# Optimization experiments

Measured on AMD Instinct MI355X. Metric: run time of the kernel, lower is better.

Reference implementation:

```python
import jax, jax.numpy as jnp
import numpy as np

NPOINT, NSAMPLE, RADIUS = 1024, 32, 0.2
EPS = 1e-5


def fps(xyz, npoint):
    # furthest point sampling: sequential over npoint steps (inherent recurrence)
    B, N, _ = xyz.shape

    def step(carry, _):
        dists, cur = carry
        last = jnp.take_along_axis(xyz, cur[:, None, None], axis=1)[:, 0]  # (B,3)
        d = jnp.sum((xyz - last[:, None, :]) ** 2, axis=-1)  # (B,N)
        dists = jnp.minimum(dists, d)
        nxt = jnp.argmax(dists, axis=-1).astype(jnp.int32)
        return (dists, nxt), cur

    init = (jnp.full((B, N), 1e10, xyz.dtype), jnp.zeros((B,), jnp.int32))
    _, idx = jax.lax.scan(step, init, None, length=npoint)
    return idx.T  # (B, npoint)


def ball_query(xyz, new_xyz, radius, nsample):
    # first `nsample` points (in index order) within radius of each query
    B, N, _ = xyz.shape
    d2 = jnp.sum((new_xyz[:, :, None, :] - xyz[:, None, :, :]) ** 2, -1)  # (B,P,N)
    mask = d2 < radius * radius
    key = jnp.where(mask, jnp.arange(N, dtype=jnp.int32), jnp.int32(N))
    negv, ord_ = jax.lax.top_k(-key, nsample)  # smallest keys = earliest valid idx
    valid = (-negv) < N
    first = ord_[..., :1]  # query point itself is always in-radius
    return jnp.where(valid, ord_, first)  # (B, P, nsample) int32


def bn_relu(x, g, b):
    # BatchNorm2d training-mode stats over (B, P, S) per channel, then ReLU
    m = jnp.mean(x, axis=(0, 1, 2))
    v = jnp.var(x, axis=(0, 1, 2))
    return jax.nn.relu((x - m) * jax.lax.rsqrt(v + EPS) * g + b)


def sa_forward(xyz, features, W1, g1, b1, W2, g2, b2, W3, g3, b3):
    B, N, _ = xyz.shape
    fps_idx = fps(xyz, NPOINT)  # (B,P)
    new_xyz = jnp.take_along_axis(xyz, fps_idx[:, :, None], axis=1)  # (B,P,3)
    idx = ball_query(xyz, new_xyz, RADIUS, NSAMPLE)  # (B,P,S)

    gather = jax.vmap(lambda pts, i: pts[i])  # per-batch irregular gather
    grouped_xyz = gather(xyz, idx) - new_xyz[:, :, None, :]  # (B,P,S,3)
    grouped_feat = gather(jnp.swapaxes(features, 1, 2), idx)  # (B,P,S,C)
    h = jnp.concatenate([grouped_xyz, grouped_feat], axis=-1)  # (B,P,S,3+C)

    # shared MLP = 1x1 Conv2d (no bias) + BN + ReLU, three layers
    h = bn_relu(jnp.einsum('bpsc,oc->bpso', h, W1), g1, b1)
    h = bn_relu(jnp.einsum('bpsc,oc->bpso', h, W2), g2, b2)
    h = bn_relu(jnp.einsum('bpsc,oc->bpso', h, W3), g3, b3)

    new_features = jnp.max(h, axis=2)  # max-pool over nsample -> (B,P,Cout)
    return new_xyz, jnp.swapaxes(new_features, 1, 2)  # (B,P,3), (B,Cout,P)


def setup_inputs() -> dict:
    key = jax.random.key(0)
    ks = jax.random.split(key, 6)
    B, N, C = 16, 4096, 64
    return {
        'xyz': jax.random.uniform(ks[0], (B, N, 3), jnp.float32),
        'features': jax.random.normal(ks[1], (B, C, N), jnp.float32),
        'W1': jax.random.normal(ks[2], (64, 67), jnp.float32) * 0.1,
        'g1': jnp.ones((64,), jnp.float32), 'b1': jnp.zeros((64,), jnp.float32),
        'W2': jax.random.normal(ks[3], (64, 64), jnp.float32) * 0.1,
        'g2': jnp.ones((64,), jnp.float32), 'b2': jnp.zeros((64,), jnp.float32),
        'W3': jax.random.normal(ks[4], (128, 64), jnp.float32) * 0.1,
        'g3': jnp.ones((128,), jnp.float32), 'b3': jnp.zeros((128,), jnp.float32),
    }


def reference(xyz, features, W1, g1, b1, W2, g2, b2, W3, g3, b3):
    return sa_forward(xyz, features, W1, g1, b1, W2, g2, b2, W3, g3, b3)
```

## Files before the change

kernel.cpp:

```cpp
#include <hip/hip_runtime.h>

#define NN 4096
#define NPOINTS 1024
#define NSAMP 32
#define MROWS (16*NPOINTS*NSAMP)
#define NPAIRS (MROWS/32)
#define OUT2_OFF (16*NPOINTS*3)
#define EPSF 1e-5f
#define RPB 128
#define NBLK 4096

typedef unsigned long long ull;
using f32x4  = __attribute__((ext_vector_type(4))) float;
using bf16x8 = __attribute__((ext_vector_type(8))) short;

__device__ __forceinline__ float bflo(unsigned int u){ union{unsigned int i; float f;} v; v.i = u << 16; return v.f; }
__device__ __forceinline__ float bfhi(unsigned int u){ union{unsigned int i; float f;} v; v.i = u & 0xffff0000u; return v.f; }
__device__ __forceinline__ unsigned short f2bf(float f){
  union{float f; unsigned int i;} v; v.f = f;
  unsigned int r = v.i + 0x7fffu + ((v.i >> 16) & 1u);
  return (unsigned short)(r >> 16);
}

__global__ __launch_bounds__(512) void k_fps(const float* __restrict__ xyz,
    float* __restrict__ nxyz, float* __restrict__ out){
  __shared__ float xs[NN], ys[NN], zs[NN];
  __shared__ ull wbest[2][8];
  const int b = blockIdx.x, t = threadIdx.x;
  const float* xb = xyz + (size_t)b*NN*3;
  for (int j = t; j < NN; j += 512){
    xs[j] = xb[j*3+0]; ys[j] = xb[j*3+1]; zs[j] = xb[j*3+2];
  }
  __syncthreads();
  float px[8], py[8], pz[8], pd[8];
  #pragma unroll
  for (int j=0;j<8;j++){ int i=j*512+t; px[j]=xs[i]; py[j]=ys[i]; pz[j]=zs[i]; pd[j]=1e10f; }
  int cur = 0;
  const int lane = t & 63, wv = t >> 6;
  for (int it=0; it<NPOINTS; ++it){
    float lx = xs[cur], ly = ys[cur], lz = zs[cur];
    if (t == 0){
      int o = (b*NPOINTS + it)*3;
      nxyz[o]=lx; nxyz[o+1]=ly; nxyz[o+2]=lz;
      out[o]=lx;  out[o+1]=ly;  out[o+2]=lz;
    }
    float bv = -1.0f; int bi = 0;
    #pragma unroll
    for (int j=0;j<8;j++){
      float dx = __fsub_rn(px[j], lx);
      float dy = __fsub_rn(py[j], ly);
      float dz = __fsub_rn(pz[j], lz);
      float d  = __fadd_rn(__fadd_rn(__fmul_rn(dx,dx), __fmul_rn(dy,dy)), __fmul_rn(dz,dz));
      float nd = fminf(pd[j], d);
      pd[j] = nd;
      if (nd > bv){ bv = nd; bi = j*512 + t; }
    }
    ull key = ((ull)__float_as_uint(bv) << 32) | (ull)(0xFFFFFFFFu - (unsigned)bi);
    #define DPPSTEP(ctrl, rmask) { \
      unsigned int tlo = __builtin_amdgcn_update_dpp(0, (int)(unsigned int)(key & 0xFFFFFFFFull), ctrl, rmask, 0xf, false); \
      unsigned int thi = __builtin_amdgcn_update_dpp(0, (int)(unsigned int)(key >> 32), ctrl, rmask, 0xf, false); \
      ull tk = ((ull)thi << 32) | (ull)tlo; \
      if (tk > key) key = tk; }
    DPPSTEP(0x111, 0xf)
    DPPSTEP(0x112, 0xf)
    DPPSTEP(0x114, 0xf)
    DPPSTEP(0x118, 0xf)
    DPPSTEP(0x142, 0xa)
    DPPSTEP(0x143, 0xc)
    #undef DPPSTEP
    if (lane == 63) wbest[it & 1][wv] = key;
    __syncthreads();
    ull best = wbest[it & 1][0];
    #pragma unroll
    for (int w=1; w<8; w++){
      ull ok = wbest[it & 1][w];
      if (ok > best) best = ok;
    }
    cur = (int)(0xFFFFFFFFu - (unsigned)(best & 0xFFFFFFFFull));
  }
}

__global__ __launch_bounds__(256) void k_ball(const float* __restrict__ xyz,
    const float* __restrict__ nxyz, int* __restrict__ ball_idx){
  const int lane = threadIdx.x & 63;
  const int q = blockIdx.x*4 + (threadIdx.x >> 6);
  const int b = q >> 10;
  const float* xb = xyz + (size_t)b*NN*3;
  const int co = q*3;
  const float cx = nxyz[co], cy = nxyz[co+1], cz = nxyz[co+2];
  const int base = q*NSAMP;
  const float R2 = 0.04f;
  int cnt = 0, first = 0;
  for (int i0 = 0; i0 < NN; i0 += 64){
    const int i = i0 + lane;
    float lx = xb[i*3+0], ly = xb[i*3+1], lz = xb[i*3+2];
    float dx = __fsub_rn(cx, lx);
    float dy = __fsub_rn(cy, ly);
    float dz = __fsub_rn(cz, lz);
    float d2 = __fadd_rn(__fadd_rn(__fmul_rn(dx,dx), __fmul_rn(dy,dy)), __fmul_rn(dz,dz));
    const bool in = (d2 < R2);
    ull mask = __ballot(in);
    if (mask){
      if (cnt == 0) first = i0 + (int)__ffsll((long long)mask) - 1;
      int slot = cnt + (int)__popcll(mask & ((1ull << lane) - 1ull));
      if (in && slot < NSAMP) ball_idx[base + slot] = i;
      cnt += (int)__popcll(mask);
      if (cnt >= NSAMP) break;
    }
  }
  if (lane >= cnt && lane < NSAMP) ball_idx[base + lane] = first;
}

__device__ __forceinline__ unsigned short packhl(float v, int isLo){
  unsigned short h = f2bf(v);
  if (isLo){ float r = __fsub_rn(v, bflo((unsigned)h)); h = f2bf(r); }
  return h;
}

__global__ __launch_bounds__(256) void k_wt(const float* __restrict__ W1, const float* __restrict__ W2,
    const float* __restrict__ W3, float* __restrict__ W1T, float* __restrict__ W2T, float* __restrict__ W3T,
    unsigned short* __restrict__ w1p, unsigned short* __restrict__ w2p, unsigned short* __restrict__ w3p){
  int t = blockIdx.x*256 + threadIdx.x;
  if (t < 67*64){ int c = t >> 6, o = t & 63;  W1T[t] = W1[o*67 + c]; }
  if (t < 64*64){ int c = t >> 6, o = t & 63;  W2T[t] = W2[o*64 + c]; }
  if (t < 64*128){ int c = t >> 7, o = t & 127; W3T[t] = W3[o*64 + c]; }
  if (t < 1024){
    int f=t>>6, l=t&63, isLo=f>>3, f0=f&7, kf=f0>>2, ntg=f0&3;
    const float* src = W1 + (ntg*16+(l&15))*67 + 3 + kf*32 + ((l>>4)*8);
    unsigned short* dst = w1p + ((size_t)f*64 + l)*8;
    #pragma unroll
    for (int j=0;j<8;j++) dst[j] = packhl(src[j], isLo);
  }
  if (t < 1024){
    int f=t>>6, l=t&63, isLo=f>>3, f0=f&7, kf=f0>>2, ntg=f0&3;
    const float* src = W2 + (ntg*16+(l&15))*64 + kf*32 + ((l>>4)*8);
    unsigned short* dst = w2p + ((size_t)f*64 + l)*8;
    #pragma unroll
    for (int j=0;j<8;j++) dst[j] = packhl(src[j], isLo);
  }
  if (t < 2048){
    int f=t>>6, l=t&63, isLo=f>>4, f0=f&15, kf=f0>>3, ntg=f0&7;
    const float* src = W3 + (ntg*16+(l&15))*64 + kf*32 + ((l>>4)*8);
    unsigned short* dst = w3p + ((size_t)f*64 + l)*8;
    #pragma unroll
    for (int j=0;j<8;j++) dst[j] = packhl(src[j], isLo);
  }
}

__global__ __launch_bounds__(256) void k_ft(const float* __restrict__ feat, unsigned short* __restrict__ featT){
  __shared__ float tile[64][65];
  const int b = blockIdx.x >> 6, n0 = (blockIdx.x & 63) << 6;
  const int t = threadIdx.x;
  const int nl = t & 63, cb = t >> 6;
  #pragma unroll
  for (int k=0;k<16;k++){
    int c = cb + (k<<2);
    tile[c][nl] = feat[((size_t)(b*64 + c))*NN + n0 + nl];
  }
  __syncthreads();
  #pragma unroll
  for (int k=0;k<16;k++){
    int nl2 = cb + (k<<2);
    featT[((size_t)(b*NN) + n0 + nl2)*64 + nl] = f2bf(tile[nl][nl2]);
  }
}

__device__ __forceinline__ void gather_y1(int r,
    const float* __restrict__ xyz, const unsigned short* __restrict__ featT,
    const float* __restrict__ nxyz, const int* __restrict__ ball_idx,
    const float* __restrict__ W1T, float* __restrict__ y)
{
  const int b = r >> 15;
  const int p = (r >> 5) & (NPOINTS-1);
  const int i = ball_idx[r];
  const int co = (b*NPOINTS + p)*3;
  const float* xp = xyz + ((size_t)(b*NN + i))*3;
  const float h0 = __fsub_rn(xp[0], nxyz[co]);
  const float h1 = __fsub_rn(xp[1], nxyz[co+1]);
  const float h2 = __fsub_rn(xp[2], nxyz[co+2]);
  #pragma unroll
  for (int o=0;o<64;o++) y[o] = h0 * W1T[o];
  #pragma unroll
  for (int o=0;o<64;o++) y[o] = fmaf(h1, W1T[64+o], y[o]);
  #pragma unroll
  for (int o=0;o<64;o++) y[o] = fmaf(h2, W1T[128+o], y[o]);
  const uint4* fp = (const uint4*)(featT + ((size_t)(b*NN + i))*64);
  #pragma unroll
  for (int c8=0;c8<8;c8++){
    const uint4 u = fp[c8];
    float fv[8];
    fv[0]=bflo(u.x); fv[1]=bfhi(u.x); fv[2]=bflo(u.y); fv[3]=bfhi(u.y);
    fv[4]=bflo(u.z); fv[5]=bfhi(u.z); fv[6]=bflo(u.w); fv[7]=bfhi(u.w);
    const float* wb = W1T + (3 + c8*8)*64;
    #pragma unroll
    for (int k=0;k<8;k++){
      #pragma unroll
      for (int o=0;o<64;o++) y[o] = fmaf(fv[k], wb[k*64+o], y[o]);
    }
  }
}

__device__ __forceinline__ void load_act(const unsigned short* __restrict__ act, int r, float* __restrict__ y){
  const uint4* p = (const uint4*)(act + (size_t)r*64);
  #pragma unroll
  for (int j=0;j<8;j++){
    uint4 u = p[j];
    y[j*8+0]=bflo(u.x); y[j*8+1]=bfhi(u.x); y[j*8+2]=bflo(u.y); y[j*8+3]=bfhi(u.y);
    y[j*8+4]=bflo(u.z); y[j*8+5]=bfhi(u.z); y[j*8+6]=bflo(u.w); y[j*8+7]=bfhi(u.w);
  }
}

__device__ __forceinline__ void store_bf16x64(unsigned short* __restrict__ dst, const float* __restrict__ y){
  uint4* row = (uint4*)dst;
  #pragma unroll
  for (int j=0;j<8;j++){
    union { uint4 u; unsigned short h[8]; } pk;
    #pragma unroll
    for (int k=0;k<8;k++) pk.h[k] = f2bf(y[j*8+k]);
    row[j] = pk.u;
  }
}

__device__ __forceinline__ void bnrelu64(float* __restrict__ y,
    const float* __restrict__ sc, const float* __restrict__ sh){
  #pragma unroll
  for (int o=0;o<64;o++) y[o] = fmaxf(0.f, fmaf(y[o], sc[o], sh[o]));
}

template<int LDW>
__device__ __forceinline__ void gemm64(const float* __restrict__ a, const float* __restrict__ WT,
                                       float* __restrict__ out){
  #pragma unroll
  for (int o=0;o<64;o++) out[o] = 0.f;
  #pragma unroll 4
  for (int c=0;c<64;c++){
    const float av = a[c];
    const float* wb = WT + c*LDW;
    #pragma unroll
    for (int o=0;o<64;o++) out[o] = fmaf(av, wb[o], out[o]);
  }
}

__device__ __forceinline__ void stats_tile(float* tile, int t, const float* __restrict__ y,
                                           float& s, float& q){
  #pragma unroll
  for (int j=0;j<64;j++) tile[t*65 + j] = y[j];
  __syncthreads();
  #pragma unroll 8
  for (int r=0;r<64;r++){
    float v = tile[r*65 + t];
    s += v; q = fmaf(v, v, q);
  }
  __syncthreads();
}

template<int STAGE, int SRC, bool STORE>
__global__ __launch_bounds__(64) void k_stage(
    const float* __restrict__ xyz, const unsigned short* __restrict__ featT,
    const float* __restrict__ nxyz, const int* __restrict__ ball_idx,
    const unsigned short* __restrict__ actin, unsigned short* __restrict__ actout,
    const float* __restrict__ W1T, const float* __restrict__ W2T, const float* __restrict__ W3T,
    const float* __restrict__ sc1, const float* __restrict__ sh1,
    const float* __restrict__ sc2, const float* __restrict__ sh2,
    float* __restrict__ sums)
{
  __shared__ float tile[64*65];
  const int t = threadIdx.x;
  float s0=0.f, q0=0.f, s1=0.f, q1=0.f;
  for (int it=0; it<RPB/64; ++it){
    const int r = blockIdx.x*RPB + it*64 + t;
    float y[64];
    if constexpr (SRC == 0) gather_y1(r, xyz, featT, nxyz, ball_idx, W1T, y);
    else                    load_act(actin, r, y);
    if constexpr (STAGE == 1){
      if constexpr (STORE) store_bf16x64(actout + (size_t)r*64, y);
      stats_tile(tile, t, y, s0, q0);
    } else if constexpr (STAGE == 2){
      bnrelu64(y, sc1, sh1);
      float y2[64];
      gemm64<64>(y, W2T, y2);
      if constexpr (STORE) store_bf16x64(actout + (size_t)r*64, y2);
      stats_tile(tile, t, y2, s0, q0);
    } else {
      float a2[64];
      if constexpr (SRC != 2){
        bnrelu64(y, sc1, sh1);
        gemm64<64>(y, W2T, a2);
      } else {
        #pragma unroll
        for (int o=0;o<64;o++) a2[o] = y[o];
      }
      bnrelu64(a2, sc2, sh2);
      float y3[64];
      gemm64<128>(a2, W3T, y3);
      if constexpr (STORE) store_bf16x64(actout + (size_t)r*128, y3);
      stats_tile(tile, t, y3, s0, q0);
      gemm64<128>(a2, W3T + 64, y3);
      if constexpr (STORE) store_bf16x64(actout + (size_t)r*128 + 64, y3);
      stats_tile(tile, t, y3, s1, q1);
    }
  }
  if constexpr (STAGE < 3){
    atomicAdd(&sums[t], s0);
    atomicAdd(&sums[64 + t], q0);
  } else {
    atomicAdd(&sums[t], s0);
    atomicAdd(&sums[64 + t], s1);
    atomicAdd(&sums[128 + t], q0);
    atomicAdd(&sums[192 + t], q1);
  }
}

template<int C>
__global__ void k_fin(const float* __restrict__ sums,
    const float* __restrict__ g, const float* __restrict__ bv,
    float* __restrict__ scale, float* __restrict__ shift)
{
  const int c = threadIdx.x;
  float m  = sums[c]   * (1.f/(float)MROWS);
  float vv = sums[C+c] * (1.f/(float)MROWS) - m*m;
  float sc = g[c] / sqrtf(vv + EPSF);
  scale[c] = sc;
  shift[c] = bv[c] - m*sc;
}

__global__ __launch_bounds__(256) void k_mg1(
    const float* __restrict__ xyz, const unsigned short* __restrict__ featT,
    const float* __restrict__ nxyz, const int* __restrict__ ball_idx,
    const unsigned short* __restrict__ w1p, const float* __restrict__ W1T,
    unsigned short* __restrict__ act1, float* __restrict__ sums)
{
  __shared__ float hxs[256], hys[256], hzs[256];
  __shared__ float w1s[192];
  __shared__ float lsum[128];
  const int t = threadIdx.x, lane = t & 63, wv = t >> 6;
  const int blkrow = blockIdx.x*256;
  {
    int r = blkrow + t;
    int b = r >> 15, p = (r >> 5) & (NPOINTS-1), i = ball_idx[r];
    const float* xp = xyz + ((size_t)(b*NN + i))*3;
    int co = (b*NPOINTS + p)*3;
    hxs[t] = __fsub_rn(xp[0], nxyz[co]);
    hys[t] = __fsub_rn(xp[1], nxyz[co+1]);
    hzs[t] = __fsub_rn(xp[2], nxyz[co+2]);
  }
  if (t < 192) w1s[t] = W1T[t];
  if (t < 128) lsum[t] = 0.f;
  __syncthreads();
  const int rowbase = blkrow + wv*64;
  const int kc0 = (lane>>4)*8;
  bf16x8 A[4][2];
  #pragma unroll
  for (int mt=0;mt<4;mt++){
    int r = rowbase + mt*16 + (lane&15);
    int b = r >> 15, i = ball_idx[r];
    const unsigned short* fp = featT + ((size_t)(b*NN + i))*64 + kc0;
    A[mt][0] = *(const bf16x8*)(fp);
    A[mt][1] = *(const bf16x8*)(fp + 32);
  }
  bf16x8 Bh[2][4], Bl[2][4];
  #pragma unroll
  for (int kf=0;kf<2;kf++)
    #pragma unroll
    for (int nt=0;nt<4;nt++){
      Bh[kf][nt] = *(const bf16x8*)(w1p + ((size_t)(kf*4+nt)*64 + lane)*8);
      Bl[kf][nt] = *(const bf16x8*)(w1p + ((size_t)(8 + kf*4+nt)*64 + lane)*8);
    }
  f32x4 c[4][4];
  const int lr0 = wv*64 + (lane>>4)*4;
  #pragma unroll
  for (int nt=0;nt<4;nt++){
    int col = nt*16 + (lane&15);
    float w0 = w1s[col], w1 = w1s[64+col], w2 = w1s[128+col];
    #pragma unroll
    for (int mt=0;mt<4;mt++)
      #pragma unroll
      for (int rr=0;rr<4;rr++){
        int lr = lr0 + mt*16 + rr;
        c[mt][nt][rr] = fmaf(hzs[lr], w2, fmaf(hys[lr], w1, hxs[lr]*w0));
      }
  }
  #pragma unroll
  for (int mt=0;mt<4;mt++)
    #pragma unroll
    for (int nt=0;nt<4;nt++){
      f32x4 acc = c[mt][nt];
      acc = __builtin_amdgcn_mfma_f32_16x16x32_bf16(A[mt][0], Bh[0][nt], acc, 0,0,0);
      acc = __builtin_amdgcn_mfma_f32_16x16x32_bf16(A[mt][1], Bh[1][nt], acc, 0,0,0);
      acc = __builtin_amdgcn_mfma_f32_16x16x32_bf16(A[mt][0], Bl[0][nt], acc, 0,0,0);
      acc = __builtin_amdgcn_mfma_f32_16x16x32_bf16(A[mt][1], Bl[1][nt], acc, 0,0,0);
      c[mt][nt] = acc;
    }
  #pragma unroll
  for (int nt=0;nt<4;nt++){
    float s=0.f, q=0.f;
    #pragma unroll
    for (int mt=0;mt<4;mt++)
      #pragma unroll
      for (int rr=0;rr<4;rr++){ float v=c[mt][nt][rr]; s+=v; q=fmaf(v,v,q); }
    s += __shfl_xor(s,16,64); s += __shfl_xor(s,32,64);
    q += __shfl_xor(q,16,64); q += __shfl_xor(q,32,64);
    if (lane<16){
      atomicAdd(&lsum[nt*16+lane], s);
      atomicAdd(&lsum[64 + nt*16+lane], q);
    }
  }
  #pragma unroll
  for (int nt=0;nt<4;nt++)
    #pragma unroll
    for (int mt=0;mt<4;mt++)
      #pragma unroll
      for (int rr=0;rr<4;rr++){
        int row = rowbase + mt*16 + (lane>>4)*4 + rr;
        act1[(size_t)row*64 + nt*16 + (lane&15)] = f2bf(c[mt][nt][rr]);
      }
  __syncthreads();
  if (t < 128) atomicAdd(&sums[t], lsum[t]);
}

__device__ __forceinline__ bf16x8 ldA_bn(const unsigned short* __restrict__ p,
    const float* __restrict__ sc, const float* __restrict__ sh){
  uint4 u = *(const uint4*)p;
  unsigned w[4] = {u.x, u.y, u.z, u.w};
  union { bf16x8 v; unsigned short h[8]; } o;
  #pragma unroll
  for (int q=0;q<4;q++){
    float lo = fmaxf(0.f, fmaf(bflo(w[q]), sc[2*q],   sh[2*q]));
    float hi = fmaxf(0.f, fmaf(bfhi(w[q]), sc[2*q+1], sh[2*q+1]));
    o.h[2*q]   = f2bf(lo);
    o.h[2*q+1] = f2bf(hi);
  }
  return o.v;
}

template<int NOUT, bool MINMAX>
__global__ __launch_bounds__(256) void k_mgemm(
    const unsigned short* __restrict__ actin,
    unsigned short* __restrict__ actout,
    const unsigned short* __restrict__ wp,
    const float* __restrict__ scp, const float* __restrict__ shp,
    float* __restrict__ sums,
    float* __restrict__ ymax, float* __restrict__ ymin)
{
  constexpr int NTG = NOUT/16;
  __shared__ float lsum[2*NOUT];
  const int t = threadIdx.x, lane = t & 63, wv = t >> 6;
  for (int i=t;i<2*NOUT;i+=256) lsum[i]=0.f;
  __syncthreads();
  const int rowbase = blockIdx.x*256 + wv*64;
  const int kc0 = (lane>>4)*8;
  float scl[16], shl[16];
  #pragma unroll
  for (int kf=0;kf<2;kf++)
    #pragma unroll
    for (int j=0;j<8;j++){
      scl[kf*8+j] = scp[kf*32+kc0+j];
      shl[kf*8+j] = shp[kf*32+kc0+j];
    }
  bf16x8 A[4][2];
  #pragma unroll
  for (int mt=0;mt<4;mt++)
    #pragma unroll
    for (int kf=0;kf<2;kf++)
      A[mt][kf] = ldA_bn(actin + ((size_t)(rowbase + mt*16 + (lane&15)))*64 + kf*32 + kc0,
                         &scl[kf*8], &shl[kf*8]);
  #pragma unroll
  for (int h=0; h<NOUT/64; h++){
    bf16x8 Bh[2][4], Bl[2][4];
    #pragma unroll
    for (int kf=0;kf<2;kf++)
      #pragma unroll
      for (int nt=0;nt<4;nt++){
        int ntg = h*4+nt;
        Bh[kf][nt] = *(const bf16x8*)(wp + ((size_t)(kf*NTG+ntg)*64 + lane)*8);
        Bl[kf][nt] = *(const bf16x8*)(wp + ((size_t)(2*NTG + kf*NTG+ntg)*64 + lane)*8);
      }
    f32x4 c[4][4];
    #pragma unroll
    for (int mt=0;mt<4;mt++)
      #pragma unroll
      for (int nt=0;nt<4;nt++){
        f32x4 acc = {0.f,0.f,0.f,0.f};
        acc = __builtin_amdgcn_mfma_f32_16x16x32_bf16(A[mt][0], Bh[0][nt], acc, 0,0,0);
        acc = __builtin_amdgcn_mfma_f32_16x16x32_bf16(A[mt][1], Bh[1][nt], acc, 0,0,0);
        acc = __builtin_amdgcn_mfma_f32_16x16x32_bf16(A[mt][0], Bl[0][nt], acc, 0,0,0);
        acc = __builtin_amdgcn_mfma_f32_16x16x32_bf16(A[mt][1], Bl[1][nt], acc, 0,0,0);
        c[mt][nt] = acc;
      }
    #pragma unroll
    for (int nt=0;nt<4;nt++){
      float s=0.f, q=0.f;
      #pragma unroll
      for (int mt=0;mt<4;mt++)
        #pragma unroll
        for (int r=0;r<4;r++){ float v=c[mt][nt][r]; s+=v; q=fmaf(v,v,q); }
      s += __shfl_xor(s,16,64); s += __shfl_xor(s,32,64);
      q += __shfl_xor(q,16,64); q += __shfl_xor(q,32,64);
      if (lane<16){
        atomicAdd(&lsum[h*64+nt*16+lane], s);
        atomicAdd(&lsum[NOUT + h*64+nt*16+lane], q);
      }
    }
    if constexpr (!MINMAX){
      #pragma unroll
      for (int nt=0;nt<4;nt++)
        #pragma unroll
        for (int mt=0;mt<4;mt++)
          #pragma unroll
          for (int r=0;r<4;r++){
            int row = rowbase + mt*16 + (lane>>4)*4 + r;
            actout[(size_t)row*NOUT + h*64 + nt*16 + (lane&15)] = f2bf(c[mt][nt][r]);
          }
    } else {
      #pragma unroll
      for (int nt=0;nt<4;nt++){
        float mx0=-1e30f, mn0=1e30f, mx1=-1e30f, mn1=1e30f;
        #pragma unroll
        for (int mt=0;mt<2;mt++)
          #pragma unroll
          for (int r=0;r<4;r++){ float v=c[mt][nt][r]; mx0=fmaxf(mx0,v); mn0=fminf(mn0,v); }
        #pragma unroll
        for (int mt=2;mt<4;mt++)
          #pragma unroll
          for (int r=0;r<4;r++){ float v=c[mt][nt][r]; mx1=fmaxf(mx1,v); mn1=fminf(mn1,v); }
        mx0=fmaxf(mx0,__shfl_xor(mx0,16,64)); mx0=fmaxf(mx0,__shfl_xor(mx0,32,64));
        mn0=fminf(mn0,__shfl_xor(mn0,16,64)); mn0=fminf(mn0,__shfl_xor(mn0,32,64));
        mx1=fmaxf(mx1,__shfl_xor(mx1,16,64)); mx1=fmaxf(mx1,__shfl_xor(mx1,32,64));
        mn1=fminf(mn1,__shfl_xor(mn1,16,64)); mn1=fminf(mn1,__shfl_xor(mn1,32,64));
        if (lane<16){
          int ch = h*64+nt*16+lane;
          int pair0 = rowbase>>5;
          float2 vx = {mx0, mx1}, vn = {mn0, mn1};
          *(float2*)(ymax + (size_t)ch*NPAIRS + pair0) = vx;
          *(float2*)(ymin + (size_t)ch*NPAIRS + pair0) = vn;
        }
      }
    }
  }
  __syncthreads();
  for (int i=t;i<2*NOUT;i+=256) atomicAdd(&sums[i], lsum[i]);
}

__global__ __launch_bounds__(256) void k_mx(const float* __restrict__ ymax,
    const float* __restrict__ ymin, const float* __restrict__ sc3,
    const float* __restrict__ sh3, float* __restrict__ out){
  int idx = blockIdx.x*256 + threadIdx.x;
  int p = idx & 1023;
  int o = (idx>>10) & 127;
  int b = idx>>17;
  float sc = sc3[o], sh = sh3[o];
  size_t src = (size_t)o*NPAIRS + b*1024 + p;
  float v = (sc >= 0.f) ? ymax[src] : ymin[src];
  out[OUT2_OFF + ((size_t)(b*128+o))*1024 + p] = fmaxf(0.f, fmaf(v, sc, sh));
}

template<bool FROMACT>
__global__ __launch_bounds__(64) void k_pass2(
    const float* __restrict__ xyz, const unsigned short* __restrict__ featT,
    const float* __restrict__ nxyz, const int* __restrict__ ball_idx,
    const unsigned short* __restrict__ act1,
    const float* __restrict__ W1T, const float* __restrict__ W2T,
    const float* __restrict__ W3,
    const float* __restrict__ sc1, const float* __restrict__ sh1,
    const float* __restrict__ sc2, const float* __restrict__ sh2,
    const float* __restrict__ sc3, const float* __restrict__ sh3,
    float* __restrict__ out)
{
  const int t = threadIdx.x;
  const int s = t & 31;
  const int pair = blockIdx.x*2 + (t >> 5);
  const int r = pair*32 + s;
  float y[64];
  if (FROMACT) load_act(act1, r, y);
  else         gather_y1(r, xyz, featT, nxyz, ball_idx, W1T, y);
  bnrelu64(y, sc1, sh1);
  float a2[64];
  gemm64<64>(y, W2T, a2);
  bnrelu64(a2, sc2, sh2);
  const int b = pair >> 10, p = pair & (NPOINTS-1);
  float* ob = out + OUT2_OFF + ((size_t)b*128)*1024 + p;
  for (int o=0;o<128;o++){
    const float* wr = W3 + o*64;
    float v = 0.f;
    #pragma unroll
    for (int c=0;c<64;c++) v = fmaf(a2[c], wr[c], v);
    v = fmaxf(0.f, fmaf(v, sc3[o], sh3[o]));
    #pragma unroll
    for (int off=16; off>=1; off>>=1) v = fmaxf(v, __shfl_xor(v, off, 64));
    if (s == 0) ob[(size_t)o*1024] = v;
  }
}

extern "C" void kernel_launch(void* const* d_in, const int* in_sizes, int n_in,
                              void* d_out, int out_size, void* d_ws, size_t ws_size,
                              hipStream_t stream) {
  const float* xyz  = (const float*)d_in[0];
  const float* feat = (const float*)d_in[1];
  const float* W1   = (const float*)d_in[2];
  const float* g1   = (const float*)d_in[3];
  const float* b1   = (const float*)d_in[4];
  const float* W2   = (const float*)d_in[5];
  const float* g2   = (const float*)d_in[6];
  const float* b2   = (const float*)d_in[7];
  const float* W3   = (const float*)d_in[8];
  const float* g3   = (const float*)d_in[9];
  const float* b3   = (const float*)d_in[10];
  float* out = (float*)d_out;
  char* ws = (char*)d_ws;

  const size_t o_nxyz = 0;
  const size_t o_ball = o_nxyz + 196608;
  const size_t o_w1t  = o_ball + 2097152;
  const size_t o_w2t  = o_w1t  + 17408;
  const size_t o_w3t  = o_w2t  + 16384;
  const size_t o_w1p  = o_w3t  + 32768;
  const size_t o_w2p  = o_w1p  + 16384;
  const size_t o_w3p  = o_w2p  + 16384;
  const size_t o_bn   = o_w3p  + 32768;
  const size_t o_sum  = o_bn   + 3072;
  const size_t o_ft   = o_sum  + 2048;
  const size_t o_mm   = o_ft   + (size_t)16*NN*64*2;
  const size_t o_act1 = o_mm   + (size_t)2*128*NPAIRS*4;
  const size_t SZ_A64 = (size_t)MROWS*64*2;
  const size_t NEED1  = o_act1 + SZ_A64;
  const size_t o_act2 = o_act1 + SZ_A64;
  const size_t NEED2  = o_act2 + SZ_A64;

  float* nxyz   = (float*)(ws + o_nxyz);
  int*   ball   = (int*)  (ws + o_ball);
  float* W1T    = (float*)(ws + o_w1t);
  float* W2T    = (float*)(ws + o_w2t);
  float* W3T    = (float*)(ws + o_w3t);
  unsigned short* w1p = (unsigned short*)(ws + o_w1p);
  unsigned short* w2p = (unsigned short*)(ws + o_w2p);
  unsigned short* w3p = (unsigned short*)(ws + o_w3p);
  float* sc1    = (float*)(ws + o_bn);
  float* sh1    = (float*)(ws + o_bn + 512);
  float* sc2    = (float*)(ws + o_bn + 1024);
  float* sh2    = (float*)(ws + o_bn + 1536);
  float* sc3    = (float*)(ws + o_bn + 2048);
  float* sh3    = (float*)(ws + o_bn + 2560);
  float* sums1  = (float*)(ws + o_sum);
  float* sums2  = (float*)(ws + o_sum + 512);
  float* sums3  = (float*)(ws + o_sum + 1024);
  unsigned short* featT = (unsigned short*)(ws + o_ft);
  float* ymax   = (float*)(ws + o_mm);
  float* ymin   = (float*)(ws + o_mm + (size_t)128*NPAIRS*4);
  unsigned short* act1  = (unsigned short*)(ws + o_act1);
  unsigned short* act2  = (unsigned short*)(ws + o_act2);

  const int tier = (ws_size >= NEED2) ? 2 : (ws_size >= NEED1) ? 1 : 0;

  hipMemsetAsync(ws + o_sum, 0, 2048, stream);

  k_wt  <<<32,   256, 0, stream>>>(W1, W2, W3, W1T, W2T, W3T, w1p, w2p, w3p);
  k_ft  <<<1024, 256, 0, stream>>>(feat, featT);
  k_fps <<<16,   512, 0, stream>>>(xyz, nxyz, out);
  k_ball<<<4096, 256, 0, stream>>>(xyz, nxyz, ball);

  if (tier == 2){
    k_mg1<<<MROWS/256, 256, 0, stream>>>(xyz, featT, nxyz, ball, w1p, W1T, act1, sums1);
    k_fin<64><<<1, 64, 0, stream>>>(sums1, g1, b1, sc1, sh1);
    k_mgemm<64,false><<<MROWS/256, 256, 0, stream>>>(act1, act2, w2p, sc1, sh1, sums2,
                                                     nullptr, nullptr);
    k_fin<64><<<1, 64, 0, stream>>>(sums2, g2, b2, sc2, sh2);
    k_mgemm<128,true><<<MROWS/256, 256, 0, stream>>>(act2, nullptr, w3p, sc2, sh2, sums3,
                                                     ymax, ymin);
    k_fin<128><<<1, 128, 0, stream>>>(sums3, g3, b3, sc3, sh3);
    k_mx<<<(16*128*1024)/256, 256, 0, stream>>>(ymax, ymin, sc3, sh3, out);
  } else if (tier == 1){
    k_stage<1,0,true><<<NBLK, 64, 0, stream>>>(xyz, featT, nxyz, ball, nullptr, act1,
                                               W1T, W2T, W3T, sc1, sh1, sc2, sh2, sums1);
    k_fin<64><<<1, 64, 0, stream>>>(sums1, g1, b1, sc1, sh1);
    k_stage<2,1,false><<<NBLK, 64, 0, stream>>>(xyz, featT, nxyz, ball, act1, nullptr,
                                                W1T, W2T, W3T, sc1, sh1, sc2, sh2, sums2);
    k_fin<64><<<1, 64, 0, stream>>>(sums2, g2, b2, sc2, sh2);
    k_stage<3,1,false><<<NBLK, 64, 0, stream>>>(xyz, featT, nxyz, ball, act1, nullptr,
                                                W1T, W2T, W3T, sc1, sh1, sc2, sh2, sums3);
    k_fin<128><<<1, 128, 0, stream>>>(sums3, g3, b3, sc3, sh3);
    k_pass2<true><<<8192, 64, 0, stream>>>(xyz, featT, nxyz, ball, act1, W1T, W2T, W3,
                                           sc1, sh1, sc2, sh2, sc3, sh3, out);
  } else {
    k_stage<1,0,false><<<NBLK, 64, 0, stream>>>(xyz, featT, nxyz, ball, nullptr, nullptr,
                                                W1T, W2T, W3T, sc1, sh1, sc2, sh2, sums1);
    k_fin<64><<<1, 64, 0, stream>>>(sums1, g1, b1, sc1, sh1);
    k_stage<2,0,false><<<NBLK, 64, 0, stream>>>(xyz, featT, nxyz, ball, nullptr, nullptr,
                                                W1T, W2T, W3T, sc1, sh1, sc2, sh2, sums2);
    k_fin<64><<<1, 64, 0, stream>>>(sums2, g2, b2, sc2, sh2);
    k_stage<3,0,false><<<NBLK, 64, 0, stream>>>(xyz, featT, nxyz, ball, nullptr, nullptr,
                                                W1T, W2T, W3T, sc1, sh1, sc2, sh2, sums3);
    k_fin<128><<<1, 128, 0, stream>>>(sums3, g3, b3, sc3, sh3);
    k_pass2<false><<<8192, 64, 0, stream>>>(xyz, featT, nxyz, ball, nullptr, W1T, W2T, W3,
                                            sc1, sh1, sc2, sh2, sc3, sh3, out);
  }
}
```

Baseline: 991.3 us.

## Merge FPS, feature transpose and weight packing into one launch

Combines the furthest-point-sampling, feature-transpose and weight-packing kernels into a single launch that dispatches on block index. The other blocks can then run alongside the 16 serial FPS blocks, removing two launches and the serialisation between them. The FPS inner loop is also reworked: it computes the per-thread max with fmaxf over paired points, then recovers the lowest matching index with equality tests, and it skips the reduction on the final iteration. The cost is a larger shared-memory footprint and 512-thread blocks for the transpose and packing work.

```diff
diff --git a/kernel.cpp b/kernel.cpp
--- a/kernel.cpp
+++ b/kernel.cpp
@@ -22,61 +22,136 @@
   return (unsigned short)(r >> 16);
 }
 
-__global__ __launch_bounds__(512) void k_fps(const float* __restrict__ xyz,
-    float* __restrict__ nxyz, float* __restrict__ out){
-  __shared__ float xs[NN], ys[NN], zs[NN];
-  __shared__ ull wbest[2][8];
-  const int b = blockIdx.x, t = threadIdx.x;
-  const float* xb = xyz + (size_t)b*NN*3;
-  for (int j = t; j < NN; j += 512){
-    xs[j] = xb[j*3+0]; ys[j] = xb[j*3+1]; zs[j] = xb[j*3+2];
-  }
-  __syncthreads();
-  float px[8], py[8], pz[8], pd[8];
-  #pragma unroll
-  for (int j=0;j<8;j++){ int i=j*512+t; px[j]=xs[i]; py[j]=ys[i]; pz[j]=zs[i]; pd[j]=1e10f; }
-  int cur = 0;
-  const int lane = t & 63, wv = t >> 6;
-  for (int it=0; it<NPOINTS; ++it){
-    float lx = xs[cur], ly = ys[cur], lz = zs[cur];
-    if (t == 0){
-      int o = (b*NPOINTS + it)*3;
-      nxyz[o]=lx; nxyz[o+1]=ly; nxyz[o+2]=lz;
-      out[o]=lx;  out[o+1]=ly;  out[o+2]=lz;
-    }
-    float bv = -1.0f; int bi = 0;
-    #pragma unroll
-    for (int j=0;j<8;j++){
-      float dx = __fsub_rn(px[j], lx);
-      float dy = __fsub_rn(py[j], ly);
-      float dz = __fsub_rn(pz[j], lz);
-      float d  = __fadd_rn(__fadd_rn(__fmul_rn(dx,dx), __fmul_rn(dy,dy)), __fmul_rn(dz,dz));
-      float nd = fminf(pd[j], d);
-      pd[j] = nd;
-      if (nd > bv){ bv = nd; bi = j*512 + t; }
-    }
-    ull key = ((ull)__float_as_uint(bv) << 32) | (ull)(0xFFFFFFFFu - (unsigned)bi);
-    #define DPPSTEP(ctrl, rmask) { \
-      unsigned int tlo = __builtin_amdgcn_update_dpp(0, (int)(unsigned int)(key & 0xFFFFFFFFull), ctrl, rmask, 0xf, false); \
-      unsigned int thi = __builtin_amdgcn_update_dpp(0, (int)(unsigned int)(key >> 32), ctrl, rmask, 0xf, false); \
-      ull tk = ((ull)thi << 32) | (ull)tlo; \
-      if (tk > key) key = tk; }
-    DPPSTEP(0x111, 0xf)
-    DPPSTEP(0x112, 0xf)
-    DPPSTEP(0x114, 0xf)
-    DPPSTEP(0x118, 0xf)
-    DPPSTEP(0x142, 0xa)
-    DPPSTEP(0x143, 0xc)
-    #undef DPPSTEP
-    if (lane == 63) wbest[it & 1][wv] = key;
+__device__ __forceinline__ unsigned short packhl(float v, int isLo){
+  unsigned short h = f2bf(v);
+  if (isLo){ float r = __fsub_rn(v, bflo((unsigned)h)); h = f2bf(r); }
+  return h;
+}
+
+__global__ __launch_bounds__(512) void k_pre(
+    const float* __restrict__ xyz, const float* __restrict__ feat,
+    const float* __restrict__ W1, const float* __restrict__ W2, const float* __restrict__ W3,
+    float* __restrict__ nxyz, float* __restrict__ out, unsigned short* __restrict__ featT,
+    float* __restrict__ W1T, float* __restrict__ W2T, float* __restrict__ W3T,
+    unsigned short* __restrict__ w1p, unsigned short* __restrict__ w2p, unsigned short* __restrict__ w3p)
+{
+  __shared__ float smem[3*NN + 64];
+  const int bid = blockIdx.x;
+  const int t = threadIdx.x;
+
+  if (bid < 16){
+    float* xs = smem; float* ys = smem + NN; float* zs = smem + 2*NN;
+    ull* wbest = (ull*)(smem + 3*NN);
+    const int b = bid;
+    const float* xb = xyz + (size_t)b*NN*3;
+    for (int j = t; j < NN; j += 512){
+      xs[j] = xb[j*3+0]; ys[j] = xb[j*3+1]; zs[j] = xb[j*3+2];
+    }
     __syncthreads();
-    ull best = wbest[it & 1][0];
-    #pragma unroll
-    for (int w=1; w<8; w++){
-      ull ok = wbest[it & 1][w];
-      if (ok > best) best = ok;
-    }
-    cur = (int)(0xFFFFFFFFu - (unsigned)(best & 0xFFFFFFFFull));
+    float2 px[4], py[4], pz[4], pd[4];
+    #pragma unroll
+    for (int j=0;j<4;j++){
+      int i0 = (2*j)*512 + t, i1 = (2*j+1)*512 + t;
+      px[j] = make_float2(xs[i0], xs[i1]);
+      py[j] = make_float2(ys[i0], ys[i1]);
+      pz[j] = make_float2(zs[i0], zs[i1]);
+      pd[j] = make_float2(1e10f, 1e10f);
+    }
+    int cur = 0;
+    const int lane = t & 63, wv = t >> 6;
+    for (int it=0; it<NPOINTS; ++it){
+      float lx = xs[cur], ly = ys[cur], lz = zs[cur];
+      if (t == 0){
+        int o = (b*NPOINTS + it)*3;
+        nxyz[o]=lx; nxyz[o+1]=ly; nxyz[o+2]=lz;
+        out[o]=lx;  out[o+1]=ly;  out[o+2]=lz;
+      }
+      if (it == NPOINTS-1) break;
+      float2 bv2 = make_float2(-1.0f, -1.0f);
+      #pragma unroll
+      for (int j=0;j<4;j++){
+        float dxx = __fsub_rn(px[j].x, lx), dxy = __fsub_rn(px[j].y, lx);
+        float dyx = __fsub_rn(py[j].x, ly), dyy = __fsub_rn(py[j].y, ly);
+        float dzx = __fsub_rn(pz[j].x, lz), dzy = __fsub_rn(pz[j].y, lz);
+        float dX = __fadd_rn(__fadd_rn(__fmul_rn(dxx,dxx), __fmul_rn(dyx,dyx)), __fmul_rn(dzx,dzx));
+        float dY = __fadd_rn(__fadd_rn(__fmul_rn(dxy,dxy), __fmul_rn(dyy,dyy)), __fmul_rn(dzy,dzy));
+        float ndX = fminf(pd[j].x, dX), ndY = fminf(pd[j].y, dY);
+        pd[j].x = ndX; pd[j].y = ndY;
+        bv2.x = fmaxf(bv2.x, ndX);
+        bv2.y = fmaxf(bv2.y, ndY);
+      }
+      float bv = fmaxf(bv2.x, bv2.y);
+      int bi = 0;
+      #pragma unroll
+      for (int j=3;j>=0;j--){
+        if (pd[j].y == bv) bi = (2*j+1)*512 + t;
+        if (pd[j].x == bv) bi = (2*j)*512 + t;
+      }
+      ull key = ((ull)__float_as_uint(bv) << 32) | (ull)(0xFFFFFFFFu - (unsigned)bi);
+      #define DPPSTEP(ctrl, rmask) { \
+        unsigned int tlo = __builtin_amdgcn_update_dpp(0, (int)(unsigned int)(key & 0xFFFFFFFFull), ctrl, rmask, 0xf, false); \
+        unsigned int thi = __builtin_amdgcn_update_dpp(0, (int)(unsigned int)(key >> 32), ctrl, rmask, 0xf, false); \
+        ull tk = ((ull)thi << 32) | (ull)tlo; \
+        if (tk > key) key = tk; }
+      DPPSTEP(0x111, 0xf)
+      DPPSTEP(0x112, 0xf)
+      DPPSTEP(0x114, 0xf)
+      DPPSTEP(0x118, 0xf)
+      DPPSTEP(0x142, 0xa)
+      DPPSTEP(0x143, 0xc)
+      #undef DPPSTEP
+      if (lane == 63) wbest[(it & 1)*8 + wv] = key;
+      __syncthreads();
+      ull best = wbest[(it & 1)*8];
+      #pragma unroll
+      for (int w=1; w<8; w++){
+        ull ok = wbest[(it & 1)*8 + w];
+        if (ok > best) best = ok;
+      }
+      cur = (int)(0xFFFFFFFFu - (unsigned)(best & 0xFFFFFFFFull));
+    }
+  } else if (bid < 16 + 1024){
+    float* tile = smem;
+    const int fb = bid - 16;
+    const int b = fb >> 6, n0 = (fb & 63) << 6;
+    const int nl = t & 63, cb = t >> 6;
+    #pragma unroll
+    for (int k=0;k<8;k++){
+      int c = cb + (k<<3);
+      tile[c*65 + nl] = feat[((size_t)(b*64 + c))*NN + n0 + nl];
+    }
+    __syncthreads();
+    #pragma unroll
+    for (int k=0;k<8;k++){
+      int nl2 = cb + (k<<3);
+      featT[((size_t)(b*NN) + n0 + nl2)*64 + nl] = f2bf(tile[nl*65 + nl2]);
+    }
+  } else {
+    int g = (bid - 1040)*512 + t;
+    if (g < 67*64){ int c = g >> 6, o = g & 63;  W1T[g] = W1[o*67 + c]; }
+    if (g < 64*64){ int c = g >> 6, o = g & 63;  W2T[g] = W2[o*64 + c]; }
+    if (g < 64*128){ int c = g >> 7, o = g & 127; W3T[g] = W3[o*64 + c]; }
+    if (g < 1024){
+      int f=g>>6, l=g&63, isLo=f>>3, f0=f&7, kf=f0>>2, ntg=f0&3;
+      const float* src = W1 + (ntg*16+(l&15))*67 + 3 + kf*32 + ((l>>4)*8);
+      unsigned short* dst = w1p + ((size_t)f*64 + l)*8;
+      #pragma unroll
+      for (int j=0;j<8;j++) dst[j] = packhl(src[j], isLo);
+    }
+    if (g < 1024){
+      int f=g>>6, l=g&63, isLo=f>>3, f0=f&7, kf=f0>>2, ntg=f0&3;
+      const float* src = W2 + (ntg*16+(l&15))*64 + kf*32 + ((l>>4)*8);
+      unsigned short* dst = w2p + ((size_t)f*64 + l)*8;
+      #pragma unroll
+      for (int j=0;j<8;j++) dst[j] = packhl(src[j], isLo);
+    }
+    if (g < 2048){
+      int f=g>>6, l=g&63, isLo=f>>4, f0=f&15, kf=f0>>3, ntg=f0&7;
+      const float* src = W3 + (ntg*16+(l&15))*64 + kf*32 + ((l>>4)*8);
+      unsigned short* dst = w3p + ((size_t)f*64 + l)*8;
+      #pragma unroll
+      for (int j=0;j<8;j++) dst[j] = packhl(src[j], isLo);
+    }
   }
 }
 
@@ -109,60 +184,6 @@
     }
   }
   if (lane >= cnt && lane < NSAMP) ball_idx[base + lane] = first;
-}
-
-__device__ __forceinline__ unsigned short packhl(float v, int isLo){
-  unsigned short h = f2bf(v);
-  if (isLo){ float r = __fsub_rn(v, bflo((unsigned)h)); h = f2bf(r); }
-  return h;
-}
-
-__global__ __launch_bounds__(256) void k_wt(const float* __restrict__ W1, const float* __restrict__ W2,
-    const float* __restrict__ W3, float* __restrict__ W1T, float* __restrict__ W2T, float* __restrict__ W3T,
-    unsigned short* __restrict__ w1p, unsigned short* __restrict__ w2p, unsigned short* __restrict__ w3p){
-  int t = blockIdx.x*256 + threadIdx.x;
-  if (t < 67*64){ int c = t >> 6, o = t & 63;  W1T[t] = W1[o*67 + c]; }
-  if (t < 64*64){ int c = t >> 6, o = t & 63;  W2T[t] = W2[o*64 + c]; }
-  if (t < 64*128){ int c = t >> 7, o = t & 127; W3T[t] = W3[o*64 + c]; }
-  if (t < 1024){
-    int f=t>>6, l=t&63, isLo=f>>3, f0=f&7, kf=f0>>2, ntg=f0&3;
-    const float* src = W1 + (ntg*16+(l&15))*67 + 3 + kf*32 + ((l>>4)*8);
-    unsigned short* dst = w1p + ((size_t)f*64 + l)*8;
-    #pragma unroll
-    for (int j=0;j<8;j++) dst[j] = packhl(src[j], isLo);
-  }
-  if (t < 1024){
-    int f=t>>6, l=t&63, isLo=f>>3, f0=f&7, kf=f0>>2, ntg=f0&3;
-    const float* src = W2 + (ntg*16+(l&15))*64 + kf*32 + ((l>>4)*8);
-    unsigned short* dst = w2p + ((size_t)f*64 + l)*8;
-    #pragma unroll
-    for (int j=0;j<8;j++) dst[j] = packhl(src[j], isLo);
-  }
-  if (t < 2048){
-    int f=t>>6, l=t&63, isLo=f>>4, f0=f&15, kf=f0>>3, ntg=f0&7;
-    const float* src = W3 + (ntg*16+(l&15))*64 + kf*32 + ((l>>4)*8);
-    unsigned short* dst = w3p + ((size_t)f*64 + l)*8;
-    #pragma unroll
-    for (int j=0;j<8;j++) dst[j] = packhl(src[j], isLo);
-  }
-}
-
-__global__ __launch_bounds__(256) void k_ft(const float* __restrict__ feat, unsigned short* __restrict__ featT){
-  __shared__ float tile[64][65];
-  const int b = blockIdx.x >> 6, n0 = (blockIdx.x & 63) << 6;
-  const int t = threadIdx.x;
-  const int nl = t & 63, cb = t >> 6;
-  #pragma unroll
-  for (int k=0;k<16;k++){
-    int c = cb + (k<<2);
-    tile[c][nl] = feat[((size_t)(b*64 + c))*NN + n0 + nl];
-  }
-  __syncthreads();
-  #pragma unroll
-  for (int k=0;k<16;k++){
-    int nl2 = cb + (k<<2);
-    featT[((size_t)(b*NN) + n0 + nl2)*64 + nl] = f2bf(tile[nl][nl2]);
-  }
 }
 
 __device__ __forceinline__ void gather_y1(int r,
@@ -653,9 +674,9 @@
 
   hipMemsetAsync(ws + o_sum, 0, 2048, stream);
 
-  k_wt  <<<32,   256, 0, stream>>>(W1, W2, W3, W1T, W2T, W3T, w1p, w2p, w3p);
-  k_ft  <<<1024, 256, 0, stream>>>(feat, featT);
-  k_fps <<<16,   512, 0, stream>>>(xyz, nxyz, out);
+  k_pre <<<16 + 1024 + 32, 512, 0, stream>>>(xyz, feat, W1, W2, W3,
+                                             nxyz, out, featT, W1T, W2T, W3T,
+                                             w1p, w2p, w3p);
   k_ball<<<4096, 256, 0, stream>>>(xyz, nxyz, ball);
 
   if (tier == 2){
```

New measurement: 1.112 ms. +12.2%, slower.

## Merge prep kernels into one launch and fold BN finalize into GEMM tails

Applied to the files above, without the earlier changes.

The weight-pack, feature-transpose and ball-query kernels become one block-indexed kernel launched after FPS. The three separate BN finalize launches are replaced by a last-block-done pattern using atomic counters inside the MLP kernels. The goal is fewer kernel launches and less launch gap on the stream. In exchange, the feature transpose now waits for FPS to finish instead of running before it, and every MLP block pays an extra threadfence and atomic.

```diff
diff --git a/kernel.cpp b/kernel.cpp
--- a/kernel.cpp
+++ b/kernel.cpp
@@ -20,6 +20,12 @@
   union{float f; unsigned int i;} v; v.f = f;
   unsigned int r = v.i + 0x7fffu + ((v.i >> 16) & 1u);
   return (unsigned short)(r >> 16);
+}
+
+__device__ __forceinline__ unsigned short packhl(float v, int isLo){
+  unsigned short h = f2bf(v);
+  if (isLo){ float r = __fsub_rn(v, bflo((unsigned)h)); h = f2bf(r); }
+  return h;
 }
 
 __global__ __launch_bounds__(512) void k_fps(const float* __restrict__ xyz,
@@ -80,88 +86,106 @@
   }
 }
 
-__global__ __launch_bounds__(256) void k_ball(const float* __restrict__ xyz,
-    const float* __restrict__ nxyz, int* __restrict__ ball_idx){
-  const int lane = threadIdx.x & 63;
-  const int q = blockIdx.x*4 + (threadIdx.x >> 6);
-  const int b = q >> 10;
-  const float* xb = xyz + (size_t)b*NN*3;
-  const int co = q*3;
-  const float cx = nxyz[co], cy = nxyz[co+1], cz = nxyz[co+2];
-  const int base = q*NSAMP;
-  const float R2 = 0.04f;
-  int cnt = 0, first = 0;
-  for (int i0 = 0; i0 < NN; i0 += 64){
-    const int i = i0 + lane;
-    float lx = xb[i*3+0], ly = xb[i*3+1], lz = xb[i*3+2];
-    float dx = __fsub_rn(cx, lx);
-    float dy = __fsub_rn(cy, ly);
-    float dz = __fsub_rn(cz, lz);
-    float d2 = __fadd_rn(__fadd_rn(__fmul_rn(dx,dx), __fmul_rn(dy,dy)), __fmul_rn(dz,dz));
-    const bool in = (d2 < R2);
-    ull mask = __ballot(in);
-    if (mask){
-      if (cnt == 0) first = i0 + (int)__ffsll((long long)mask) - 1;
-      int slot = cnt + (int)__popcll(mask & ((1ull << lane) - 1ull));
-      if (in && slot < NSAMP) ball_idx[base + slot] = i;
-      cnt += (int)__popcll(mask);
-      if (cnt >= NSAMP) break;
-    }
-  }
-  if (lane >= cnt && lane < NSAMP) ball_idx[base + lane] = first;
-}
-
-__device__ __forceinline__ unsigned short packhl(float v, int isLo){
-  unsigned short h = f2bf(v);
-  if (isLo){ float r = __fsub_rn(v, bflo((unsigned)h)); h = f2bf(r); }
-  return h;
-}
-
-__global__ __launch_bounds__(256) void k_wt(const float* __restrict__ W1, const float* __restrict__ W2,
-    const float* __restrict__ W3, float* __restrict__ W1T, float* __restrict__ W2T, float* __restrict__ W3T,
-    unsigned short* __restrict__ w1p, unsigned short* __restrict__ w2p, unsigned short* __restrict__ w3p){
-  int t = blockIdx.x*256 + threadIdx.x;
-  if (t < 67*64){ int c = t >> 6, o = t & 63;  W1T[t] = W1[o*67 + c]; }
-  if (t < 64*64){ int c = t >> 6, o = t & 63;  W2T[t] = W2[o*64 + c]; }
-  if (t < 64*128){ int c = t >> 7, o = t & 127; W3T[t] = W3[o*64 + c]; }
-  if (t < 1024){
-    int f=t>>6, l=t&63, isLo=f>>3, f0=f&7, kf=f0>>2, ntg=f0&3;
-    const float* src = W1 + (ntg*16+(l&15))*67 + 3 + kf*32 + ((l>>4)*8);
-    unsigned short* dst = w1p + ((size_t)f*64 + l)*8;
-    #pragma unroll
-    for (int j=0;j<8;j++) dst[j] = packhl(src[j], isLo);
-  }
-  if (t < 1024){
-    int f=t>>6, l=t&63, isLo=f>>3, f0=f&7, kf=f0>>2, ntg=f0&3;
-    const float* src = W2 + (ntg*16+(l&15))*64 + kf*32 + ((l>>4)*8);
-    unsigned short* dst = w2p + ((size_t)f*64 + l)*8;
-    #pragma unroll
-    for (int j=0;j<8;j++) dst[j] = packhl(src[j], isLo);
-  }
-  if (t < 2048){
-    int f=t>>6, l=t&63, isLo=f>>4, f0=f&15, kf=f0>>3, ntg=f0&7;
-    const float* src = W3 + (ntg*16+(l&15))*64 + kf*32 + ((l>>4)*8);
-    unsigned short* dst = w3p + ((size_t)f*64 + l)*8;
-    #pragma unroll
-    for (int j=0;j<8;j++) dst[j] = packhl(src[j], isLo);
-  }
-}
-
-__global__ __launch_bounds__(256) void k_ft(const float* __restrict__ feat, unsigned short* __restrict__ featT){
-  __shared__ float tile[64][65];
-  const int b = blockIdx.x >> 6, n0 = (blockIdx.x & 63) << 6;
+__global__ __launch_bounds__(256) void k_pb(
+    const float* __restrict__ xyz, const float* __restrict__ nxyz, int* __restrict__ ball_idx,
+    const float* __restrict__ feat, unsigned short* __restrict__ featT,
+    const float* __restrict__ W1, const float* __restrict__ W2, const float* __restrict__ W3,
+    float* __restrict__ W1T, float* __restrict__ W2T, float* __restrict__ W3T,
+    unsigned short* __restrict__ w1p, unsigned short* __restrict__ w2p, unsigned short* __restrict__ w3p)
+{
+  __shared__ float tile[64*65];
+  const int bid = blockIdx.x;
   const int t = threadIdx.x;
-  const int nl = t & 63, cb = t >> 6;
-  #pragma unroll
-  for (int k=0;k<16;k++){
-    int c = cb + (k<<2);
-    tile[c][nl] = feat[((size_t)(b*64 + c))*NN + n0 + nl];
-  }
-  __syncthreads();
-  #pragma unroll
-  for (int k=0;k<16;k++){
-    int nl2 = cb + (k<<2);
-    featT[((size_t)(b*NN) + n0 + nl2)*64 + nl] = f2bf(tile[nl][nl2]);
+  if (bid < 1024){
+    const int b = bid >> 6, n0 = (bid & 63) << 6;
+    const int nl = t & 63, cb = t >> 6;
+    #pragma unroll
+    for (int k=0;k<16;k++){
+      int c = cb + (k<<2);
+      tile[c*65 + nl] = feat[((size_t)(b*64 + c))*NN + n0 + nl];
+    }
+    __syncthreads();
+    #pragma unroll
+    for (int k=0;k<16;k++){
+      int nl2 = cb + (k<<2);
+      featT[((size_t)(b*NN) + n0 + nl2)*64 + nl] = f2bf(tile[nl*65 + nl2]);
+    }
+  } else if (bid < 1056){
+    int g = (bid - 1024)*256 + t;
+    if (g < 67*64){ int c = g >> 6, o = g & 63;  W1T[g] = W1[o*67 + c]; }
+    if (g < 64*64){ int c = g >> 6, o = g & 63;  W2T[g] = W2[o*64 + c]; }
+    if (g < 64*128){ int c = g >> 7, o = g & 127; W3T[g] = W3[o*64 + c]; }
+    if (g < 1024){
+      int f=g>>6, l=g&63, isLo=f>>3, f0=f&7, kf=f0>>2, ntg=f0&3;
+      const float* src = W1 + (ntg*16+(l&15))*67 + 3 + kf*32 + ((l>>4)*8);
+      unsigned short* dst = w1p + ((size_t)f*64 + l)*8;
+      #pragma unroll
+      for (int j=0;j<8;j++) dst[j] = packhl(src[j], isLo);
+    }
+    if (g < 1024){
+      int f=g>>6, l=g&63, isLo=f>>3, f0=f&7, kf=f0>>2, ntg=f0&3;
+      const float* src = W2 + (ntg*16+(l&15))*64 + kf*32 + ((l>>4)*8);
+      unsigned short* dst = w2p + ((size_t)f*64 + l)*8;
+      #pragma unroll
+      for (int j=0;j<8;j++) dst[j] = packhl(src[j], isLo);
+    }
+    if (g < 2048){
+      int f=g>>6, l=g&63, isLo=f>>4, f0=f&15, kf=f0>>3, ntg=f0&7;
+      const float* src = W3 + (ntg*16+(l&15))*64 + kf*32 + ((l>>4)*8);
+      unsigned short* dst = w3p + ((size_t)f*64 + l)*8;
+      #pragma unroll
+      for (int j=0;j<8;j++) dst[j] = packhl(src[j], isLo);
+    }
+  } else {
+    const int lane = t & 63;
+    const int q = (bid - 1056)*4 + (t >> 6);
+    const int b = q >> 10;
+    const float* xb = xyz + (size_t)b*NN*3;
+    const int co = q*3;
+    const float cx = nxyz[co], cy = nxyz[co+1], cz = nxyz[co+2];
+    const int base = q*NSAMP;
+    const float R2 = 0.04f;
+    int cnt = 0, first = 0;
+    for (int i0 = 0; i0 < NN; i0 += 64){
+      const int i = i0 + lane;
+      float lx = xb[i*3+0], ly = xb[i*3+1], lz = xb[i*3+2];
+      float dx = __fsub_rn(cx, lx);
+      float dy = __fsub_rn(cy, ly);
+      float dz = __fsub_rn(cz, lz);
+      float d2 = __fadd_rn(__fadd_rn(__fmul_rn(dx,dx), __fmul_rn(dy,dy)), __fmul_rn(dz,dz));
+      const bool in = (d2 < R2);
+      ull mask = __ballot(in);
+      if (mask){
+        if (cnt == 0) first = i0 + (int)__ffsll((long long)mask) - 1;
+        int slot = cnt + (int)__popcll(mask & ((1ull << lane) - 1ull));
+        if (in && slot < NSAMP) ball_idx[base + slot] = i;
+        cnt += (int)__popcll(mask);
+        if (cnt >= NSAMP) break;
+      }
+    }
+    if (lane >= cnt && lane < NSAMP) ball_idx[base + lane] = first;
+  }
+}
+
+template<int C>
+__device__ __forceinline__ void fin_lastblock(float* __restrict__ sums,
+    unsigned int* __restrict__ cnt, const float* __restrict__ g,
+    const float* __restrict__ bvec, float* __restrict__ scale,
+    float* __restrict__ shift, int t, int nblocks)
+{
+  __shared__ int isLast;
+  __threadfence();
+  __syncthreads();
+  if (t == 0) isLast = (atomicAdd(cnt, 1u) == (unsigned)(nblocks - 1));
+  __syncthreads();
+  if (isLast && t < C){
+    float s  = atomicAdd(&sums[t], 0.f);
+    float qq = atomicAdd(&sums[C + t], 0.f);
+    float m  = s  * (1.f/(float)MROWS);
+    float vv = qq * (1.f/(float)MROWS) - m*m;
+    float sc = g[t] / sqrtf(vv + EPSF);
+    scale[t] = sc;
+    shift[t] = bvec[t] - m*sc;
   }
 }
 
@@ -328,7 +352,9 @@
     const float* __restrict__ xyz, const unsigned short* __restrict__ featT,
     const float* __restrict__ nxyz, const int* __restrict__ ball_idx,
     const unsigned short* __restrict__ w1p, const float* __restrict__ W1T,
-    unsigned short* __restrict__ act1, float* __restrict__ sums)
+    unsigned short* __restrict__ act1, float* __restrict__ sums,
+    unsigned int* __restrict__ cnt, const float* __restrict__ g1,
+    const float* __restrict__ b1, float* __restrict__ sc1, float* __restrict__ sh1)
 {
   __shared__ float hxs[256], hys[256], hzs[256];
   __shared__ float w1s[192];
@@ -416,6 +442,7 @@
       }
   __syncthreads();
   if (t < 128) atomicAdd(&sums[t], lsum[t]);
+  fin_lastblock<64>(sums, cnt, g1, b1, sc1, sh1, t, gridDim.x);
 }
 
 __device__ __forceinline__ bf16x8 ldA_bn(const unsigned short* __restrict__ p,
@@ -440,7 +467,9 @@
     const unsigned short* __restrict__ wp,
     const float* __restrict__ scp, const float* __restrict__ shp,
     float* __restrict__ sums,
-    float* __restrict__ ymax, float* __restrict__ ymin)
+    float* __restrict__ ymax, float* __restrict__ ymin,
+    unsigned int* __restrict__ cnt, const float* __restrict__ g,
+    const float* __restrict__ bvec, float* __restrict__ scale, float* __restrict__ shift)
 {
   constexpr int NTG = NOUT/16;
   __shared__ float lsum[2*NOUT];
@@ -539,6 +568,7 @@
   }
   __syncthreads();
   for (int i=t;i<2*NOUT;i+=256) atomicAdd(&sums[i], lsum[i]);
+  fin_lastblock<NOUT>(sums, cnt, g, bvec, scale, shift, t, gridDim.x);
 }
 
 __global__ __launch_bounds__(256) void k_mx(const float* __restrict__ ymax,
@@ -618,7 +648,7 @@
   const size_t o_w3p  = o_w2p  + 16384;
   const size_t o_bn   = o_w3p  + 32768;
   const size_t o_sum  = o_bn   + 3072;
-  const size_t o_ft   = o_sum  + 2048;
+  const size_t o_ft   = o_sum  + 2112;
   const size_t o_mm   = o_ft   + (size_t)16*NN*64*2;
   const size_t o_act1 = o_mm   + (size_t)2*128*NPAIRS*4;
   const size_t SZ_A64 = (size_t)MROWS*64*2;
@@ -643,6 +673,9 @@
   float* sums1  = (float*)(ws + o_sum);
   float* sums2  = (float*)(ws + o_sum + 512);
   float* sums3  = (float*)(ws + o_sum + 1024);
+  unsigned int* cnt1 = (unsigned int*)(ws + o_sum + 2048);
+  unsigned int* cnt2 = (unsigned int*)(ws + o_sum + 2052);
+  unsigned int* cnt3 = (unsigned int*)(ws + o_sum + 2056);
   unsigned short* featT = (unsigned short*)(ws + o_ft);
   float* ymax   = (float*)(ws + o_mm);
   float* ymin   = (float*)(ws + o_mm + (size_t)128*NPAIRS*4);
@@ -651,22 +684,19 @@
 
   const int tier = (ws_size >= NEED2) ? 2 : (ws_size >= NEED1) ? 1 : 0;
 
-  hipMemsetAsync(ws + o_sum, 0, 2048, stream);
-
-  k_wt  <<<32,   256, 0, stream>>>(W1, W2, W3, W1T, W2T, W3T, w1p, w2p, w3p);
-  k_ft  <<<1024, 256, 0, stream>>>(feat, featT);
-  k_fps <<<16,   512, 0, stream>>>(xyz, nxyz, out);
-  k_ball<<<4096, 256, 0, stream>>>(xyz, nxyz, ball);
+  hipMemsetAsync(ws + o_sum, 0, 2112, stream);
+
+  k_fps<<<16, 512, 0, stream>>>(xyz, nxyz, out);
+  k_pb <<<1056 + 4096, 256, 0, stream>>>(xyz, nxyz, ball, feat, featT,
+                                         W1, W2, W3, W1T, W2T, W3T, w1p, w2p, w3p);
 
   if (tier == 2){
-    k_mg1<<<MROWS/256, 256, 0, stream>>>(xyz, featT, nxyz, ball, w1p, W1T, act1, sums1);
-    k_fin<64><<<1, 64, 0, stream>>>(sums1, g1, b1, sc1, sh1);
+    k_mg1<<<MROWS/256, 256, 0, stream>>>(xyz, featT, nxyz, ball, w1p, W1T, act1, sums1,
+                                         cnt1, g1, b1, sc1, sh1);
     k_mgemm<64,false><<<MROWS/256, 256, 0, stream>>>(act1, act2, w2p, sc1, sh1, sums2,
-                                                     nullptr, nullptr);
-    k_fin<64><<<1, 64, 0, stream>>>(sums2, g2, b2, sc2, sh2);
+                                                     nullptr, nullptr, cnt2, g2, b2, sc2, sh2);
     k_mgemm<128,true><<<MROWS/256, 256, 0, stream>>>(act2, nullptr, w3p, sc2, sh2, sums3,
-                                                     ymax, ymin);
-    k_fin<128><<<1, 128, 0, stream>>>(sums3, g3, b3, sc3, sh3);
+                                                     ymax, ymin, cnt3, g3, b3, sc3, sh3);
     k_mx<<<(16*128*1024)/256, 256, 0, stream>>>(ymax, ymin, sc3, sh3, out);
   } else if (tier == 1){
     k_stage<1,0,true><<<NBLK, 64, 0, stream>>>(xyz, featT, nxyz, ball, nullptr, act1,
```

After: 1.718 ms. 73.3% more time.
